# Kernel tuning notes

Measured on AMD Instinct MI355X. Metric: run time of the kernel, lower is better.

Reference implementation:

```python
import jax, jax.numpy as jnp
import numpy as np

B, L, C = 8, 512, 6        # graphs per batch, nodes per graph, atom channels
N = B * L
BOS = 0                    # global-node token id
ATOM_POS_PAD = 0           # atom position pad idx
BIGINT = 1e10

def setup_inputs() -> dict:
    key = jax.random.key(0)
    k1, k2, k3, k4 = jax.random.split(key, 4)
    X = jax.random.normal(k1, (N, C, 3), dtype=jnp.float32) * 5.0
    AP = jax.random.randint(k2, (N, C), 0, 8)              # 0 == atom_pos pad
    S = jax.random.randint(k3, (N,), 1, 16)
    S = S.at[jnp.arange(B) * L].set(BOS)                    # first node of each graph is BOS/global
    sec_pos = jax.random.randint(k4, (N,), 0, 4)
    batch_id = jnp.repeat(jnp.arange(B), L)
    return {"X": X, "AP": AP, "S": S, "sec_pos": sec_pos, "batch_id": batch_id, "k": 9}

def _knn_dist(X, AP, S):
    # per-graph pairwise node distance = min over atom-channel pairs of ||x_ic - x_jd||
    Xb = X.reshape(B, L, C, 3)
    sq = jnp.sum(Xb * Xb, axis=-1)                               # [B,L,C]
    dots = jnp.einsum('bicx,bjdx->bijcd', Xb, Xb)                # [B,L,L,C,C]
    d2 = sq[:, :, None, :, None] + sq[:, None, :, None, :] - 2.0 * dots
    dist = jnp.sqrt(jnp.maximum(d2, 0.0))
    pad = (AP.reshape(B, L, C) == ATOM_POS_PAD)
    pair_pad = pad[:, :, None, :, None] | pad[:, None, :, None, :]
    dist = dist + pair_pad.astype(dist.dtype) * BIGINT
    dist = jnp.min(dist.reshape(B, L, L, C * C), axis=-1)       # [B,L,L]
    # kNN only over non-global (not BOS) endpoints
    glb = (S.reshape(B, L) == BOS)
    gmask = glb[:, :, None] | glb[:, None, :]
    return jnp.where(gmask, jnp.asarray(BIGINT, dist.dtype), dist)

def reference(X, AP, S, sec_pos, batch_id, k):
    dist = _knn_dist(X, AP, S)
    neg_d, dst_local = jax.lax.top_k(-dist, k)                   # smallest-k per row, [B,L,k]
    dknn = (-neg_d).reshape(N, k)
    offs = jnp.arange(B) * L                                      # per-graph node offsets
    dst = (dst_local + offs[:, None, None]).reshape(N, k)
    src = jnp.broadcast_to(jnp.arange(N)[:, None], (N, k))
    valid = dknn < BIGINT
    valid = valid & (sec_pos[src] == sec_pos[dst])               # sec_pos[row]==sec_pos[col] filter
    dst = jnp.where(valid, dst, -1)                              # invalid edges marked -1 (static shape)
    # global edges: (0,j) for all j plus (i,0) for i>=1, per graph
    g_src_l = jnp.concatenate([jnp.zeros(L, jnp.int32), jnp.arange(1, L)])
    g_dst_l = jnp.concatenate([jnp.arange(L), jnp.zeros(L - 1, jnp.int32)])
    glb_edges = jnp.stack([
        (g_src_l[None, :] + offs[:, None]).reshape(-1),
        (g_dst_l[None, :] + offs[:, None]).reshape(-1)])
    # sequential edges among non-global nodes: |i-j|==1, i,j>=1
    a = jnp.arange(1, L - 1)
    s_src_l = jnp.concatenate([a, a + 1])
    s_dst_l = jnp.concatenate([a + 1, a])
    seq_edges = jnp.stack([
        (s_src_l[None, :] + offs[:, None]).reshape(-1),
        (s_dst_l[None, :] + offs[:, None]).reshape(-1)])
    return dknn, src, dst, valid, glb_edges, seq_edges
```

## Files before the change

### kernel.cpp

```cpp
#include <hip/hip_runtime.h>

#define B_  8
#define L_  512
#define C_  6
#define N_  (B_ * L_)
#define K_  9
#define BIGF 1e10f

#define NK        (N_ * K_)
#define OFF_DKNN  0
#define OFF_SRC   (NK)
#define OFF_DST   (2 * NK)
#define OFF_VALID (3 * NK)
#define OFF_GLB   (4 * NK)
#define GLB_PER   (2 * L_ - 1)
#define GLB_TOT   (2 * B_ * GLB_PER)
#define OFF_SEQ   (OFF_GLB + GLB_TOT)
#define SEQ_PER   (2 * (L_ - 2))
#define SEQ_TOT   (2 * B_ * SEQ_PER)

#define TPB 512
#define RPB 8

static __device__ __forceinline__ unsigned umin32(unsigned a, unsigned b) {
    return a < b ? a : b;
}

__global__ __launch_bounds__(TPB, 4) void fused_kernel(const float* __restrict__ X,
                                                       const int* __restrict__ AP,
                                                       const int* __restrict__ S,
                                                       const int* __restrict__ sec,
                                                       float* __restrict__ out) {
    __shared__ float4 ch[C_][L_];

    const int tid = threadIdx.x;
    const int lane = tid & 63;
    const int wv = tid >> 6;
    const int row = blockIdx.x * RPB + wv;
    const int base = row & ~(L_ - 1);
    const int rl = row & (L_ - 1);

    {
        const int gt = blockIdx.x * TPB + tid;
        if (gt < GLB_TOT) {
            const int r = gt / (B_ * GLB_PER);
            const int rem = gt % (B_ * GLB_PER);
            const int b = rem / GLB_PER;
            const int q = rem % GLB_PER;
            int v;
            if (r == 0) v = (q < L_) ? 0 : (q - (L_ - 1));
            else        v = (q < L_) ? q : 0;
            out[OFF_GLB + gt] = (float)(v + b * L_);
        }
        if (gt < SEQ_TOT) {
            const int r = gt / (B_ * SEQ_PER);
            const int rem = gt % (B_ * SEQ_PER);
            const int b = rem / SEQ_PER;
            const int q = rem % SEQ_PER;
            int v;
            if (r == 0) v = (q < L_ - 2) ? (q + 1) : (q - (L_ - 2) + 2);
            else        v = (q < L_ - 2) ? (q + 2) : (q - (L_ - 2) + 1);
            out[OFF_SEQ + gt] = (float)(v + b * L_);
        }
    }

    {
        const int node = base + tid;
        const float* x = X + (size_t)node * (C_ * 3);
        const float bias_g = (S[node] == 0) ? BIGF : 0.0f;
#pragma unroll
        for (int c = 0; c < C_; ++c) {
            const float a = x[c * 3], b = x[c * 3 + 1], d = x[c * 3 + 2];
            float sq = (a * a + b * b) + d * d;
            if (AP[node * C_ + c] == 0) sq += BIGF;
            ch[c][tid] = make_float4(a, b, d, sq + bias_g);
        }
    }
    __syncthreads();

    float ax[C_], ay[C_], az[C_], sc[C_];
#pragma unroll
    for (int c = 0; c < C_; ++c) {
        const float4 q = ch[c][rl];
        ax[c] = -2.0f * q.x; ay[c] = -2.0f * q.y; az[c] = -2.0f * q.z;
        sc[c] = q.w;
    }

    unsigned v[8];
#pragma unroll
    for (int s = 0; s < 8; ++s) {
        const int col = s * 64 + lane;
        float m = 3.0e38f;
#pragma unroll
        for (int d = 0; d < C_; ++d) {
            const float4 q = ch[d][col];
            float md = 3.0e38f;
#pragma unroll
            for (int c = 0; c < C_; ++c) {
                const float val = fmaf(az[c], q.z, fmaf(ay[c], q.y, fmaf(ax[c], q.x, sc[c])));
                md = fminf(md, val);
            }
            m = fminf(m, md + q.w);
        }
        m = fmaxf(m, 0.0f);
        v[s] = (__float_as_uint(m) & 0xFFFFFE00u) | (unsigned)col;
    }

    unsigned mine = 0xFFFFFFFFu;
#pragma unroll
    for (int t = 0; t < K_; ++t) {
        unsigned loc = v[0];
#pragma unroll
        for (int s = 1; s < 8; ++s) loc = umin32(loc, v[s]);
#pragma unroll
        for (int off = 32; off >= 1; off >>= 1) {
            const unsigned o = (unsigned)__shfl_xor((int)loc, off, 64);
            loc = umin32(loc, o);
        }
        if (lane == t) mine = loc;
#pragma unroll
        for (int s = 0; s < 8; ++s)
            v[s] = (v[s] == loc) ? 0xFFFFFFFFu : v[s];
    }

    if (lane < K_) {
        const int col = (int)(mine & 511u);
        const float d2 = __uint_as_float(mine & 0xFFFFFE00u);
        const bool masked = (d2 >= 1.0e9f);
        const float dval = masked ? BIGF : sqrtf(d2);
        const int dst = base + col;
        const bool valid = !masked && (sec[row] == sec[dst]);
        const size_t o = (size_t)row * K_ + lane;
        out[OFF_DKNN + o]  = dval;
        out[OFF_SRC + o]   = (float)row;
        out[OFF_DST + o]   = valid ? (float)dst : -1.0f;
        out[OFF_VALID + o] = valid ? 1.0f : 0.0f;
    }
}

extern "C" void kernel_launch(void* const* d_in, const int* in_sizes, int n_in,
                              void* d_out, int out_size, void* d_ws, size_t ws_size,
                              hipStream_t stream) {
    (void)in_sizes; (void)n_in; (void)out_size; (void)d_ws; (void)ws_size;
    const float* X   = (const float*)d_in[0];
    const int*   AP  = (const int*)d_in[1];
    const int*   S   = (const int*)d_in[2];
    const int*   sec = (const int*)d_in[3];
    float* out = (float*)d_out;

    hipLaunchKernelGGL(fused_kernel, dim3(N_ / RPB), dim3(TPB), 0, stream,
                       X, AP, S, sec, out);
}
```

Measured before the change: 72.96 us.

## Hold column atoms in registers, broadcast row atoms, use packed FMA

Each thread now owns one column node and keeps its six atom coordinates in packed float2 registers. It loops over the block's 8 rows, loading row atoms as uniform broadcasts, and computes the pair distances with packed v2f FMA and min operations. Results go through a per-row shared buffer for the existing wave top-k selection. This removes the per-column float4 LDS reads in the inner loop and enables dual-issue packed math. In exchange it adds redundant global loads of row data and an extra LDS round trip.

```diff
diff --git a/kernel.cpp b/kernel.cpp
--- a/kernel.cpp
+++ b/kernel.cpp
@@ -22,6 +22,8 @@
 #define TPB 512
 #define RPB 8
 
+typedef float v2f __attribute__((ext_vector_type(2)));
+
 static __device__ __forceinline__ unsigned umin32(unsigned a, unsigned b) {
     return a < b ? a : b;
 }
@@ -31,14 +33,14 @@
                                                        const int* __restrict__ S,
                                                        const int* __restrict__ sec,
                                                        float* __restrict__ out) {
-    __shared__ float4 ch[C_][L_];
+    __shared__ unsigned kbuf[RPB][L_];
 
     const int tid = threadIdx.x;
     const int lane = tid & 63;
     const int wv = tid >> 6;
-    const int row = blockIdx.x * RPB + wv;
-    const int base = row & ~(L_ - 1);
-    const int rl = row & (L_ - 1);
+    const int row0 = blockIdx.x * RPB;
+    const int gbase = row0 & ~(L_ - 1);
+    const int mycol = (wv << 6) | lane;
 
     {
         const int gt = blockIdx.x * TPB + tid;
@@ -64,47 +66,78 @@
         }
     }
 
+    v2f cmx[3], cmy[3], cmz[3], csq[3];
     {
-        const int node = base + tid;
-        const float* x = X + (size_t)node * (C_ * 3);
-        const float bias_g = (S[node] == 0) ? BIGF : 0.0f;
+        const int cnode = gbase + mycol;
+        const float* xc = X + (size_t)cnode * 18;
+        float cx[C_], cy[C_], cz[C_];
+        float2 h[9];
+#pragma unroll
+        for (int i = 0; i < 9; ++i) h[i] = ((const float2*)xc)[i];
+        const float* hf = (const float*)h;
 #pragma unroll
         for (int c = 0; c < C_; ++c) {
-            const float a = x[c * 3], b = x[c * 3 + 1], d = x[c * 3 + 2];
-            float sq = (a * a + b * b) + d * d;
-            if (AP[node * C_ + c] == 0) sq += BIGF;
-            ch[c][tid] = make_float4(a, b, d, sq + bias_g);
+            cx[c] = hf[c * 3]; cy[c] = hf[c * 3 + 1]; cz[c] = hf[c * 3 + 2];
         }
+        const float bias_g = (S[cnode] == 0) ? BIGF : 0.0f;
+        float cq[C_];
+#pragma unroll
+        for (int c = 0; c < C_; ++c) {
+            float sq = (cx[c] * cx[c] + cy[c] * cy[c]) + cz[c] * cz[c];
+            if (AP[cnode * C_ + c] == 0) sq += BIGF;
+            cq[c] = sq + bias_g;
+        }
+#pragma unroll
+        for (int p = 0; p < 3; ++p) {
+            cmx[p] = (v2f){-2.0f * cx[2 * p], -2.0f * cx[2 * p + 1]};
+            cmy[p] = (v2f){-2.0f * cy[2 * p], -2.0f * cy[2 * p + 1]};
+            cmz[p] = (v2f){-2.0f * cz[2 * p], -2.0f * cz[2 * p + 1]};
+            csq[p] = (v2f){cq[2 * p], cq[2 * p + 1]};
+        }
+    }
+
+#pragma unroll
+    for (int r = 0; r < RPB; ++r) {
+        const int rnode = row0 + r;
+        const float* xr = X + (size_t)rnode * 18;
+        const float rbias = (S[rnode] == 0) ? BIGF : 0.0f;
+        float rx[C_], ry[C_], rz[C_], rq[C_];
+#pragma unroll
+        for (int c = 0; c < C_; ++c) {
+            rx[c] = xr[c * 3]; ry[c] = xr[c * 3 + 1]; rz[c] = xr[c * 3 + 2];
+            float sq = (rx[c] * rx[c] + ry[c] * ry[c]) + rz[c] * rz[c];
+            if (AP[rnode * C_ + c] == 0) sq += BIGF;
+            rq[c] = sq + rbias;
+        }
+        v2f md[3] = {(v2f)(3.0e38f), (v2f)(3.0e38f), (v2f)(3.0e38f)};
+#pragma unroll
+        for (int c = 0; c < C_; ++c) {
+            const v2f seed = (v2f){rq[c], rq[c]};
+            const v2f sx = (v2f){rx[c], rx[c]};
+            const v2f sy = (v2f){ry[c], ry[c]};
+            const v2f sz = (v2f){rz[c], rz[c]};
+#pragma unroll
+            for (int p = 0; p < 3; ++p) {
+                v2f t = __builtin_elementwise_fma(sx, cmx[p], seed);
+                t = __builtin_elementwise_fma(sy, cmy[p], t);
+                t = __builtin_elementwise_fma(sz, cmz[p], t);
+                md[p] = __builtin_elementwise_min(md[p], t);
+            }
+        }
+        float m = 3.0e38f;
+#pragma unroll
+        for (int p = 0; p < 3; ++p) {
+            const v2f ms = md[p] + csq[p];
+            m = fminf(m, fminf(ms.x, ms.y));
+        }
+        m = fmaxf(m, 0.0f);
+        kbuf[r][mycol] = (__float_as_uint(m) & 0xFFFFFE00u) | (unsigned)mycol;
     }
     __syncthreads();
 
-    float ax[C_], ay[C_], az[C_], sc[C_];
-#pragma unroll
-    for (int c = 0; c < C_; ++c) {
-        const float4 q = ch[c][rl];
-        ax[c] = -2.0f * q.x; ay[c] = -2.0f * q.y; az[c] = -2.0f * q.z;
-        sc[c] = q.w;
-    }
-
     unsigned v[8];
 #pragma unroll
-    for (int s = 0; s < 8; ++s) {
-        const int col = s * 64 + lane;
-        float m = 3.0e38f;
-#pragma unroll
-        for (int d = 0; d < C_; ++d) {
-            const float4 q = ch[d][col];
-            float md = 3.0e38f;
-#pragma unroll
-            for (int c = 0; c < C_; ++c) {
-                const float val = fmaf(az[c], q.z, fmaf(ay[c], q.y, fmaf(ax[c], q.x, sc[c])));
-                md = fminf(md, val);
-            }
-            m = fminf(m, md + q.w);
-        }
-        m = fmaxf(m, 0.0f);
-        v[s] = (__float_as_uint(m) & 0xFFFFFE00u) | (unsigned)col;
-    }
+    for (int s = 0; s < 8; ++s) v[s] = kbuf[wv][s * 64 + lane];
 
     unsigned mine = 0xFFFFFFFFu;
 #pragma unroll
@@ -124,11 +157,12 @@
     }
 
     if (lane < K_) {
+        const int row = row0 + wv;
         const int col = (int)(mine & 511u);
         const float d2 = __uint_as_float(mine & 0xFFFFFE00u);
         const bool masked = (d2 >= 1.0e9f);
         const float dval = masked ? BIGF : sqrtf(d2);
-        const int dst = base + col;
+        const int dst = gbase + col;
         const bool valid = !masked && (sec[row] == sec[dst]);
         const size_t o = (size_t)row * K_ + lane;
         out[OFF_DKNN + o]  = dval;
```

New measurement: 74.88 us. +2.6%, slower.
